# Optimization experiments

Hardware: AMD Instinct MI355X
Metric: run time of the kernel (lower is better)

## Reference

```python
import jax, jax.numpy as jnp
import numpy as np

K = 4
EDGE_NUM = 8978
SLOPE = 0.33


def _add_self_loops(ei, w, n):
    # add_self_loops(..., fill_value=-1.0); inputs assumed already coalesced
    loop = jnp.arange(n, dtype=ei.dtype)
    src = jnp.concatenate([ei[0], loop])
    dst = jnp.concatenate([ei[1], loop])
    w = jnp.concatenate([w, jnp.full((n,), -1.0, w.dtype)])
    return src, dst, w


def _cheb_bn_lrelu(x, src, dst, w, theta, bias, gamma, beta):
    # HodgeChebConv (PyG ChebConv recurrence) + BatchNorm + LeakyReLU; dropout = eval/no-op
    n = x.shape[0]

    def prop(z):  # y[dst] += w * z[src]
        return jax.ops.segment_sum(w[:, None] * z[src], dst, num_segments=n)

    Tx0 = x
    out = jnp.einsum('ni,io->no', Tx0, theta[0])
    Tx1 = prop(Tx0)
    out = out + jnp.einsum('ni,io->no', Tx1, theta[1])
    for k in range(2, K):
        Tx2 = 2.0 * prop(Tx1) - Tx0
        out = out + jnp.einsum('ni,io->no', Tx2, theta[k])
        Tx0, Tx1 = Tx1, Tx2
    out = out + bias
    mu = out.mean(0)
    var = out.var(0)
    out = (out - mu) * jax.lax.rsqrt(var + 1e-5) * gamma + beta
    return jnp.where(out >= 0, out, SLOPE * out)


def _bn(x, g, b):
    mu = x.mean(0)
    var = x.var(0)
    return (x - mu) * jax.lax.rsqrt(var + 1e-5) * g + b


def setup_inputs() -> dict:
    key = jax.random.key(0)
    ks = jax.random.split(key, 16)
    f32 = jnp.float32
    B = 64
    N = B * EDGE_NUM
    N2 = N // 2
    E = N * 8
    E1 = N2 * 8
    inp = {}
    inp['x_s'] = jax.random.normal(ks[0], (N, 1), f32)
    inp['edge_index_s'] = jax.random.randint(ks[1], (2, E), 0, N)
    inp['edge_weight_s'] = jax.random.normal(ks[2], (E,), f32) * 0.1
    inp['edge_index_s1'] = jax.random.randint(ks[3], (2, E1), 0, N2)
    inp['edge_weight_s1'] = jax.random.normal(ks[4], (E1,), f32) * 0.1
    # graclus-style pairing of node matchings (deterministic stand-in)
    inp['cluster'] = jnp.arange(N, dtype=jnp.int32) // 2
    inp['theta0'] = jax.random.normal(ks[5], (K, 1, 32), f32) * 0.1
    inp['bias0'] = jnp.zeros((32,), f32)
    inp['gamma0'] = jnp.ones((32,), f32)
    inp['beta0'] = jnp.zeros((32,), f32)
    inp['theta1'] = jax.random.normal(ks[6], (K, 32, 32), f32) * 0.1
    inp['bias1'] = jnp.zeros((32,), f32)
    inp['gamma1'] = jnp.ones((32,), f32)
    inp['beta1'] = jnp.zeros((32,), f32)
    inp['theta2'] = jax.random.normal(ks[7], (K, 32, 1), f32) * 0.1
    inp['bias2'] = jnp.zeros((1,), f32)
    inp['gamma2'] = jnp.ones((1,), f32)
    inp['beta2'] = jnp.zeros((1,), f32)
    LIN_IN = EDGE_NUM // 2  # 4489
    inp['W1'] = jax.random.normal(ks[8], (LIN_IN, 256), f32) * 0.02
    inp['b1'] = jnp.zeros((256,), f32)
    inp['g1'] = jnp.ones((256,), f32)
    inp['be1'] = jnp.zeros((256,), f32)
    inp['W2'] = jax.random.normal(ks[9], (256, 128), f32) * 0.05
    inp['b2'] = jnp.zeros((128,), f32)
    inp['g2'] = jnp.ones((128,), f32)
    inp['be2'] = jnp.zeros((128,), f32)
    inp['W3'] = jax.random.normal(ks[10], (128, 1), f32) * 0.05
    inp['b3'] = jnp.zeros((1,), f32)
    return inp


def reference(x_s, edge_weight_s, edge_weight_s1, theta0, bias0, gamma0, beta0,
              theta1, bias1, gamma1, beta1, theta2, bias2, gamma2, beta2,
              W1, b1, g1, be1, W2, b2, g2, be2, W3, b3,
              edge_index_s, edge_index_s1, cluster):
    n = x_s.shape[0]
    batch = n // EDGE_NUM
    n2 = n // 2
    src, dst, w = _add_self_loops(edge_index_s, edge_weight_s, n)
    x = _cheb_bn_lrelu(x_s, src, dst, w, theta0, bias0, gamma0, beta0)
    # Graclus max-pool with externally supplied cluster assignment + pooled graph
    x = jax.ops.segment_max(x, cluster, num_segments=n2)
    src1, dst1, w1 = _add_self_loops(edge_index_s1, edge_weight_s1, n2)
    x = _cheb_bn_lrelu(x, src1, dst1, w1, theta1, bias1, gamma1, beta1)
    x = _cheb_bn_lrelu(x, src1, dst1, w1, theta2, bias2, gamma2, beta2)
    x = x.reshape(batch, -1)  # [B, edge_num/2] since last channel = 1
    x = jax.nn.relu(_bn(x @ W1 + b1, g1, be1))
    x = jax.nn.relu(_bn(x @ W2 + b2, g2, be2))
    return x @ W3 + b3
```

## Files before the change

kernel.cpp:

```cpp
#include <hip/hip_runtime.h>

#define TPB 256
#define PBLK 512
#define BSH 12
#define BKT 4096
#define PCH 2048

__global__ __launch_bounds__(256) void bcount_k(const int* __restrict__ dst,
                                                int* __restrict__ bcnt, int NB, int E) {
  __shared__ int h[256];
  int tid = threadIdx.x;
  h[tid] = 0;
  __syncthreads();
  int stride = gridDim.x * 256;
  for (int e = blockIdx.x * 256 + tid; e < E; e += stride) atomicAdd(&h[dst[e] >> BSH], 1);
  __syncthreads();
  if (tid < NB && h[tid]) atomicAdd(&bcnt[tid], h[tid]);
}

__global__ void bscan_k(const int* __restrict__ bcnt, int* __restrict__ bbase,
                        int* __restrict__ bcur, int NB) {
  __shared__ int ls[256];
  int tid = threadIdx.x;
  int v = (tid < NB) ? bcnt[tid] : 0;
  ls[tid] = v;
  __syncthreads();
  for (int off = 1; off < 256; off <<= 1) {
    int t = (tid >= off) ? ls[tid - off] : 0;
    __syncthreads();
    ls[tid] += t;
    __syncthreads();
  }
  if (tid < NB) {
    bbase[tid] = ls[tid] - v;
    bcur[tid] = ls[tid] - v;
  }
}

__global__ __launch_bounds__(256) void bpart_k(const int* __restrict__ src,
                                               const int* __restrict__ dst,
                                               const float* __restrict__ w, int* __restrict__ gcur,
                                               int* __restrict__ psrc, int* __restrict__ pw,
                                               int* __restrict__ pdst, int NB, int E) {
  __shared__ int hist[256], start[256], resv[256], lcur[256];
  __shared__ int s_src[PCH], s_w[PCH], s_dst[PCH];
  __shared__ int total;
  int tid = threadIdx.x;
  int base = blockIdx.x * PCH;
  hist[tid] = 0;
  __syncthreads();
  int es[8], ds[8], wsv[8], bs[8];
#pragma unroll
  for (int i = 0; i < 8; ++i) {
    int e = base + i * 256 + tid;
    bool v = e < E;
    ds[i] = v ? dst[e] : 0;
    es[i] = v ? src[e] : 0;
    wsv[i] = v ? __float_as_int(w[e]) : 0;
    bs[i] = v ? (ds[i] >> BSH) : -1;
    if (v) atomicAdd(&hist[bs[i]], 1);
  }
  __syncthreads();
  int hv = hist[tid];
  start[tid] = hv;
  __syncthreads();
  for (int off = 1; off < 256; off <<= 1) {
    int t = (tid >= off) ? start[tid - off] : 0;
    __syncthreads();
    start[tid] += t;
    __syncthreads();
  }
  int ex = start[tid] - hv;
  __syncthreads();
  start[tid] = ex;
  lcur[tid] = ex;
  if (tid == 255) total = ex + hv;
  if (tid < NB && hv) resv[tid] = atomicAdd(&gcur[tid], hv);
  __syncthreads();
#pragma unroll
  for (int i = 0; i < 8; ++i) {
    if (bs[i] >= 0) {
      int p = atomicAdd(&lcur[bs[i]], 1);
      s_src[p] = es[i];
      s_w[p] = wsv[i];
      s_dst[p] = ds[i];
    }
  }
  __syncthreads();
  int m = total;
  for (int i = tid; i < m; i += 256) {
    int d = s_dst[i];
    int b = d >> BSH;
    int g = resv[b] + (i - start[b]);
    psrc[g] = s_src[i];
    pw[g] = s_w[i];
    pdst[g] = d;
  }
}

__global__ __launch_bounds__(1024) void bbuild_k(const int* __restrict__ psrc,
                                                 const int* __restrict__ pw,
                                                 const int* __restrict__ pdst,
                                                 const int* __restrict__ bbase,
                                                 const int* __restrict__ bcnt,
                                                 int* __restrict__ rowptr, int2* __restrict__ csw,
                                                 int n, int NB, int Etot) {
  __shared__ int hist[BKT];
  __shared__ int cur[BKT];
  __shared__ int aux[1024];
  int tid = threadIdx.x;
  int b = blockIdx.x;
  int node0 = b << BSH;
  int nn = min(BKT, n - node0);
  for (int i = tid; i < BKT; i += 1024) hist[i] = 0;
  __syncthreads();
  int ebase = bbase[b], ecnt = bcnt[b];
  for (int i = tid; i < ecnt; i += 1024) atomicAdd(&hist[pdst[ebase + i] - node0], 1);
  __syncthreads();
  int h0 = hist[tid * 4], h1 = hist[tid * 4 + 1], h2 = hist[tid * 4 + 2], h3 = hist[tid * 4 + 3];
  int s = h0 + h1 + h2 + h3;
  aux[tid] = s;
  __syncthreads();
  for (int off = 1; off < 1024; off <<= 1) {
    int t = (tid >= off) ? aux[tid - off] : 0;
    __syncthreads();
    aux[tid] += t;
    __syncthreads();
  }
  int ex = aux[tid] - s;
  hist[tid * 4] = ex;
  hist[tid * 4 + 1] = ex + h0;
  hist[tid * 4 + 2] = ex + h0 + h1;
  hist[tid * 4 + 3] = ex + h0 + h1 + h2;
  cur[tid * 4] = ex;
  cur[tid * 4 + 1] = ex + h0;
  cur[tid * 4 + 2] = ex + h0 + h1;
  cur[tid * 4 + 3] = ex + h0 + h1 + h2;
  __syncthreads();
  for (int j = tid; j < nn; j += 1024) rowptr[node0 + j] = ebase + hist[j];
  if (b == NB - 1 && tid == 0) rowptr[n] = Etot;
  for (int i = tid; i < ecnt; i += 1024) {
    int d = pdst[ebase + i] - node0;
    int p = atomicAdd(&cur[d], 1);
    csw[ebase + p] = make_int2(psrc[ebase + i], pw[ebase + i]);
  }
}

__global__ __launch_bounds__(256) void gather_s_k(float* __restrict__ out,
                                                  const float* __restrict__ z,
                                                  const float* __restrict__ bsub, float cb,
                                                  const int* __restrict__ rowptr,
                                                  const int2* __restrict__ csw, float scale,
                                                  int n) {
  int t = blockIdx.x * TPB + threadIdx.x;
  int node = t >> 3, q = t & 7;
  if (node >= n) return;
  int beg = rowptr[node], deg = rowptr[node + 1] - beg;
  float part = 0.f;
  for (int jb = 0; jb < deg; jb += 8) {
    int j = jb + q;
    int2 e = csw[beg + (j < deg ? j : 0)];
    int sj = (j < deg) ? e.x : 0;
    float zv = z[sj];
    part += (j < deg) ? __int_as_float(e.y) * zv : 0.f;
  }
  part += __shfl_xor(part, 1, 8);
  part += __shfl_xor(part, 2, 8);
  part += __shfl_xor(part, 4, 8);
  if (q == 0) out[node] = scale * (part - z[node]) + cb * bsub[node];
}

__global__ __launch_bounds__(256) void cheb0_fused_k(float4* __restrict__ out,
                                                     const float* __restrict__ x,
                                                     const float* __restrict__ t1,
                                                     const float* __restrict__ t2,
                                                     const int* __restrict__ rowptr,
                                                     const int2* __restrict__ csw,
                                                     const float* __restrict__ th ,
                                                     const float* __restrict__ bias, int n) {
  int t = blockIdx.x * TPB + threadIdx.x;
  int node = t >> 3, q = t & 7;
  if (node >= n) return;
  int beg = rowptr[node], deg = rowptr[node + 1] - beg;
  float part = 0.f;
  for (int jb = 0; jb < deg; jb += 8) {
    int j = jb + q;
    int2 e = csw[beg + (j < deg ? j : 0)];
    int sj = (j < deg) ? e.x : 0;
    float zv = t2[sj];
    part += (j < deg) ? __int_as_float(e.y) * zv : 0.f;
  }
  part += __shfl_xor(part, 1, 8);
  part += __shfl_xor(part, 2, 8);
  part += __shfl_xor(part, 4, 8);
  float t2n = t2[node], t1n = t1[node], xn = x[node];
  float t3 = 2.f * (part - t2n) - t1n;
  const float4* th4 = (const float4*)th;
  float4 a0 = th4[q], a1 = th4[8 + q], a2 = th4[16 + q], a3 = th4[24 + q];
  float4 b = ((const float4*)bias)[q];
  float4 r;
  r.x = xn * a0.x + t1n * a1.x + t2n * a2.x + t3 * a3.x + b.x;
  r.y = xn * a0.y + t1n * a1.y + t2n * a2.y + t3 * a3.y + b.y;
  r.z = xn * a0.z + t1n * a1.z + t2n * a2.z + t3 * a3.z + b.z;
  r.w = xn * a0.w + t1n * a1.w + t2n * a2.w + t3 * a3.w + b.w;
  out[(size_t)node * 8 + q] = r;
}

__device__ __forceinline__ float4 gather_row8(const float4* __restrict__ z,
                                              const int* __restrict__ rowptr,
                                              const int2* __restrict__ csw, int node, int q) {
  int beg = rowptr[node], deg = rowptr[node + 1] - beg;
  int full = min(deg, 8);
  int2 e = csw[beg + (q < deg ? q : 0)];
  int sj[8];
  float wj[8];
#pragma unroll
  for (int j = 0; j < 8; ++j) {
    int s = __shfl(e.x, j, 8);
    float w = __int_as_float(__shfl(e.y, j, 8));
    sj[j] = (j < full) ? s : 0;
    wj[j] = (j < full) ? w : 0.f;
  }
  float4 v[8];
#pragma unroll
  for (int j = 0; j < 8; ++j) v[j] = z[(size_t)sj[j] * 8 + q];
  float4 acc = {0.f, 0.f, 0.f, 0.f};
#pragma unroll
  for (int j = 0; j < 8; ++j) {
    acc.x = fmaf(wj[j], v[j].x, acc.x);
    acc.y = fmaf(wj[j], v[j].y, acc.y);
    acc.z = fmaf(wj[j], v[j].z, acc.z);
    acc.w = fmaf(wj[j], v[j].w, acc.w);
  }
  for (int j = 8; j < deg; ++j) {
    int2 ee = csw[beg + j];
    float w = __int_as_float(ee.y);
    float4 vv = z[(size_t)ee.x * 8 + q];
    acc.x = fmaf(w, vv.x, acc.x);
    acc.y = fmaf(w, vv.y, acc.y);
    acc.z = fmaf(w, vv.z, acc.z);
    acc.w = fmaf(w, vv.w, acc.w);
  }
  return acc;
}

__global__ __launch_bounds__(256) void gather_v32_k(float4* __restrict__ out,
                                                    const float4* __restrict__ z,
                                                    const float4* __restrict__ bsub, float cb,
                                                    const int* __restrict__ rowptr,
                                                    const int2* __restrict__ csw, float scale,
                                                    int n) {
  int t = blockIdx.x * TPB + threadIdx.x;
  int node = t >> 3, q = t & 7;
  if (node >= n) return;
  float4 acc = gather_row8(z, rowptr, csw, node, q);
  float4 zn = z[(size_t)node * 8 + q];
  float4 r;
  r.x = scale * (acc.x - zn.x);
  r.y = scale * (acc.y - zn.y);
  r.z = scale * (acc.z - zn.z);
  r.w = scale * (acc.w - zn.w);
  if (cb != 0.f) {
    float4 bs = bsub[(size_t)node * 8 + q];
    r.x = fmaf(cb, bs.x, r.x);
    r.y = fmaf(cb, bs.y, r.y);
    r.z = fmaf(cb, bs.z, r.z);
    r.w = fmaf(cb, bs.w, r.w);
  }
  out[(size_t)node * 8 + q] = r;
}

__global__ __launch_bounds__(256) void cheb32_fused_k(
    float4* __restrict__ out, const float4* __restrict__ x0, const float4* __restrict__ x1,
    const float4* __restrict__ x2, const int* __restrict__ rowptr, const int2* __restrict__ csw,
    const float* __restrict__ th , const float* __restrict__ bias, int n) {
  __shared__ float sth[4096];
  __shared__ float sx[4][32][36];
  int tid = threadIdx.x;
  for (int i = tid; i < 4096; i += 256) sth[i] = th[i];
  int t = blockIdx.x * TPB + tid;
  int node = t >> 3, q = t & 7, ln = tid >> 3;
  if (node < n) {
    float4 acc = gather_row8(x2, rowptr, csw, node, q);
    float4 tb = x2[(size_t)node * 8 + q];
    float4 ta = x1[(size_t)node * 8 + q];
    float4 xi = x0[(size_t)node * 8 + q];
    float4 tc;
    tc.x = 2.f * (acc.x - tb.x) - ta.x;
    tc.y = 2.f * (acc.y - tb.y) - ta.y;
    tc.z = 2.f * (acc.z - tb.z) - ta.z;
    tc.w = 2.f * (acc.w - tb.w) - ta.w;
    *(float4*)&sx[0][ln][q * 4] = xi;
    *(float4*)&sx[1][ln][q * 4] = ta;
    *(float4*)&sx[2][ln][q * 4] = tb;
    *(float4*)&sx[3][ln][q * 4] = tc;
  }
  __syncthreads();
  if (node < n) {
    float4 r = ((const float4*)bias)[q];
#pragma unroll
    for (int k = 0; k < 4; ++k) {
      const float* xr = sx[k][ln];
      const float* tr = &sth[k * 1024 + q * 4];
#pragma unroll
      for (int i = 0; i < 32; ++i) {
        float xv = xr[i];
        float4 tv = *(const float4*)&tr[i * 32];
        r.x = fmaf(xv, tv.x, r.x);
        r.y = fmaf(xv, tv.y, r.y);
        r.z = fmaf(xv, tv.z, r.z);
        r.w = fmaf(xv, tv.w, r.w);
      }
    }
    out[(size_t)node * 8 + q] = r;
  }
}

__global__ __launch_bounds__(256) void cheb1_fused_k(
    float* __restrict__ out, const float4* __restrict__ x0, const float4* __restrict__ x1,
    const float4* __restrict__ x2, const int* __restrict__ rowptr, const int2* __restrict__ csw,
    const float* __restrict__ th , const float* __restrict__ bias, int n) {
  int t = blockIdx.x * TPB + threadIdx.x;
  int node = t >> 3, q = t & 7;
  if (node >= n) return;
  float4 acc = gather_row8(x2, rowptr, csw, node, q);
  float4 tb = x2[(size_t)node * 8 + q];
  float4 ta = x1[(size_t)node * 8 + q];
  float4 xi = x0[(size_t)node * 8 + q];
  float4 tc;
  tc.x = 2.f * (acc.x - tb.x) - ta.x;
  tc.y = 2.f * (acc.y - tb.y) - ta.y;
  tc.z = 2.f * (acc.z - tb.z) - ta.z;
  tc.w = 2.f * (acc.w - tb.w) - ta.w;
  const float4* th4 = (const float4*)th;
  float4 h0 = th4[q], h1 = th4[8 + q], h2 = th4[16 + q], h3 = th4[24 + q];
  float p = xi.x * h0.x + xi.y * h0.y + xi.z * h0.z + xi.w * h0.w;
  p += ta.x * h1.x + ta.y * h1.y + ta.z * h1.z + ta.w * h1.w;
  p += tb.x * h2.x + tb.y * h2.y + tb.z * h2.z + tb.w * h2.w;
  p += tc.x * h3.x + tc.y * h3.y + tc.z * h3.z + tc.w * h3.w;
  p += __shfl_xor(p, 1);
  p += __shfl_xor(p, 2);
  p += __shfl_xor(p, 4);
  if (q == 0) out[node] = p + bias[0];
}

__global__ void bnlr_pool_k(float* __restrict__ y, const float* __restrict__ x,
                            const float* __restrict__ mv, const float* __restrict__ g,
                            const float* __restrict__ be, int n2c, float slope) {
  int i = blockIdx.x * TPB + threadIdx.x;
  if (i < n2c) {
    int p = i >> 5, c = i & 31;
    float sc = mv[32 + c] * g[c];
    float sh = be[c] - mv[c] * sc;
    float a = x[(size_t)(2 * p) * 32 + c] * sc + sh;
    float b = x[(size_t)(2 * p + 1) * 32 + c] * sc + sh;
    a = a >= 0.f ? a : slope * a;
    b = b >= 0.f ? b : slope * b;
    y[i] = fmaxf(a, b);
  }
}

__global__ __launch_bounds__(256) void stats_k(const float* __restrict__ x,
                                               float* __restrict__ partial, int C, int total) {
  float s = 0.f, q = 0.f;
  int stride = gridDim.x * TPB;
  for (int i = blockIdx.x * TPB + threadIdx.x; i < total; i += stride) {
    float v = x[i];
    s += v;
    q += v * v;
  }
  __shared__ float ss[256], sq[256];
  int tid = threadIdx.x;
  ss[tid] = s;
  sq[tid] = q;
  __syncthreads();
  for (int st = 128; st >= C; st >>= 1) {
    if (tid < st) {
      ss[tid] += ss[tid + st];
      sq[tid] += sq[tid + st];
    }
    __syncthreads();
  }
  if (tid < C) {
    partial[blockIdx.x * 2 * C + tid] = ss[tid];
    partial[blockIdx.x * 2 * C + C + tid] = sq[tid];
  }
}

__global__ __launch_bounds__(1024) void stats_fin_k(const float* __restrict__ partial,
                                                    float* __restrict__ mv, int C, int nblk,
                                                    float invR) {
  __shared__ float ss[1024], sq[1024];
  int tid = threadIdx.x;
  int G = 1024 / C;
  int g = tid / C, c = tid - g * C;
  float s = 0.f, q = 0.f;
  for (int b = g; b < nblk; b += G) {
    s += partial[b * 2 * C + c];
    q += partial[b * 2 * C + C + c];
  }
  ss[tid] = s;
  sq[tid] = q;
  __syncthreads();
  for (int st = 512; st >= C; st >>= 1) {
    if (tid < st) {
      ss[tid] += ss[tid + st];
      sq[tid] += sq[tid + st];
    }
    __syncthreads();
  }
  if (tid < C) {
    float mu = ss[tid] * invR;
    float var = sq[tid] * invR - mu * mu;
    mv[tid] = mu;
    mv[C + tid] = rsqrtf(var + 1e-5f);
  }
}

__global__ void bn_lrelu_k(float* __restrict__ y, const float* __restrict__ mv,
                           const float* __restrict__ g, const float* __restrict__ be, int C,
                           int total, float slope) {
  int i = blockIdx.x * TPB + threadIdx.x;
  if (i < total) {
    int c = i & (C - 1);
    float v = (y[i] - mv[c]) * mv[C + c] * g[c] + be[c];
    y[i] = v >= 0.f ? v : slope * v;
  }
}

__global__ void mlp1_init_k(float* __restrict__ h, const float* __restrict__ bias) {
  int i = blockIdx.x * TPB + threadIdx.x;
  h[i] = bias[i & 255];
}

#define MS 32
__global__ __launch_bounds__(256) void mlp1_split_k(const float* __restrict__ x,
                                                    const float* __restrict__ W,
                                                    float* __restrict__ h, int LIN) {
  int bb = blockIdx.x * 8;
  int s = blockIdx.y;
  int chunk = (LIN + MS - 1) / MS;
  int k0 = s * chunk;
  int k1 = min(k0 + chunk, LIN);
  __shared__ float sx[8][144];
  for (int i = threadIdx.x; i < 8 * chunk; i += 256) {
    int r = i / chunk, k = i - r * chunk;
    sx[r][k] = (k0 + k < LIN) ? x[(size_t)(bb + r) * LIN + k0 + k] : 0.f;
  }
  __syncthreads();
  int o = threadIdx.x;
  float acc[8] = {0.f, 0.f, 0.f, 0.f, 0.f, 0.f, 0.f, 0.f};
  for (int k = k0; k < k1; ++k) {
    float wv = W[(size_t)k * 256 + o];
#pragma unroll
    for (int r = 0; r < 8; ++r) acc[r] = fmaf(sx[r][k - k0], wv, acc[r]);
  }
#pragma unroll
  for (int r = 0; r < 8; ++r) unsafeAtomicAdd(&h[(bb + r) * 256 + o], acc[r]);
}

__global__ void bn_relu64_k(float* __restrict__ h, const float* __restrict__ g,
                            const float* __restrict__ be, int C, int R) {
  int c = blockIdx.x * blockDim.x + threadIdx.x;
  if (c < C) {
    float s = 0.f, q = 0.f;
    for (int r = 0; r < R; ++r) {
      float v = h[r * C + c];
      s += v;
      q += v * v;
    }
    float mu = s / R;
    float inv = rsqrtf(q / R - mu * mu + 1e-5f);
    for (int r = 0; r < R; ++r) {
      float v = (h[r * C + c] - mu) * inv * g[c] + be[c];
      h[r * C + c] = v > 0.f ? v : 0.f;
    }
  }
}

__global__ void mlp2_k(const float* __restrict__ x, const float* __restrict__ W,
                       const float* __restrict__ bias, float* __restrict__ h, int IN, int OUT) {
  __shared__ float sx[256];
  int b = blockIdx.x;
  for (int i = threadIdx.x; i < IN; i += blockDim.x) sx[i] = x[b * IN + i];
  __syncthreads();
  int o = threadIdx.x;
  if (o < OUT) {
    float acc = 0.f;
    for (int i = 0; i < IN; ++i) acc = fmaf(sx[i], W[i * OUT + o], acc);
    h[b * OUT + o] = acc + bias[o];
  }
}

__global__ void mlp3_k(const float* __restrict__ x, const float* __restrict__ W,
                       const float* __restrict__ b3, float* __restrict__ out, int IN, int B) {
  int b = threadIdx.x;
  if (b < B) {
    float acc = 0.f;
    for (int i = 0; i < IN; ++i) acc = fmaf(x[b * IN + i], W[i], acc);
    out[b] = acc + b3[0];
  }
}

extern "C" void kernel_launch(void* const* d_in, const int* in_sizes, int n_in, void* d_out,
                              int out_size, void* d_ws, size_t ws_size, hipStream_t stream) {
  const float* x_s = (const float*)d_in[0];
  const int* ei = (const int*)d_in[1];
  const float* ew = (const float*)d_in[2];
  const int* ei1 = (const int*)d_in[3];
  const float* ew1 = (const float*)d_in[4];
  const float* th0 = (const float*)d_in[6];
  const float* cb0 = (const float*)d_in[7];
  const float* g0 = (const float*)d_in[8];
  const float* be0 = (const float*)d_in[9];
  const float* th1 = (const float*)d_in[10];
  const float* cb1 = (const float*)d_in[11];
  const float* g1c = (const float*)d_in[12];
  const float* be1c = (const float*)d_in[13];
  const float* th2 = (const float*)d_in[14];
  const float* cb2 = (const float*)d_in[15];
  const float* g2c = (const float*)d_in[16];
  const float* be2c = (const float*)d_in[17];
  const float* W1 = (const float*)d_in[18];
  const float* mb1 = (const float*)d_in[19];
  const float* mg1 = (const float*)d_in[20];
  const float* mbe1 = (const float*)d_in[21];
  const float* W2 = (const float*)d_in[22];
  const float* mb2 = (const float*)d_in[23];
  const float* mg2 = (const float*)d_in[24];
  const float* mbe2 = (const float*)d_in[25];
  const float* W3 = (const float*)d_in[26];
  const float* mb3 = (const float*)d_in[27];
  float* outp = (float*)d_out;

  const int N = in_sizes[0];
  const int E = in_sizes[2];
  const int N2 = N / 2;
  const int E1 = in_sizes[4];
  const int B = out_size;
  const int LIN = N2 / B;
  const size_t NC = (size_t)N * 32, N2C = (size_t)N2 * 32;

  const int* srcA = ei;
  const int* dstA = ei + E;
  const int* src1 = ei1;
  const int* dst1 = ei1 + E1;

  float* ws = (float*)d_ws;
  float* OUT0 = ws;
  float* X1 = OUT0 + NC;
  float* TA = X1 + N2C;
  float* TB = TA + N2C;
  float* OUT1 = TB + N2C;
  int* deg1 = (int*)(OUT1 + N2C);
  int* rowptr1 = deg1 + N2;
  int2* csw1 = (int2*)(rowptr1 + N2 + 2);
  float* partial = (float*)(csw1 + E1);
  float* mv = partial + PBLK * 64;
  int* bcnt = (int*)(mv + 64);
  int* bbase = bcnt + 256;
  int* bcur = bbase + 256;
  float* h1 = (float*)(bcur + 256);
  float* h2 = h1 + (size_t)B * 256;
  int* psrc = (int*)OUT0;
  int* pw = psrc + E;
  int* pdst = pw + E;
  int2* csw0 = (int2*)X1;
  float* t1 = TA;
  int* rowptr0 = (int*)TA + N;
  float* t2 = TB;
  float* OUT2 = X1;

  auto cdiv = [](long long a, long long b) { return (unsigned)((a + b - 1) / b); };
  int NB0 = (int)cdiv(N, BKT), NB1 = (int)cdiv(N2, BKT);

  hipMemsetAsync(bcnt, 0, 256 * 4, stream);
  bcount_k<<<1024, 256, 0, stream>>>(dstA, bcnt, NB0, E);
  bscan_k<<<1, 256, 0, stream>>>(bcnt, bbase, bcur, NB0);
  bpart_k<<<cdiv(E, PCH), 256, 0, stream>>>(srcA, dstA, ew, bcur, psrc, pw, pdst, NB0, E);
  bbuild_k<<<NB0, 1024, 0, stream>>>(psrc, pw, pdst, bbase, bcnt, rowptr0, csw0, N, NB0, E);

  hipMemsetAsync(bcnt, 0, 256 * 4, stream);
  bcount_k<<<1024, 256, 0, stream>>>(dst1, bcnt, NB1, E1);
  bscan_k<<<1, 256, 0, stream>>>(bcnt, bbase, bcur, NB1);
  bpart_k<<<cdiv(E1, PCH), 256, 0, stream>>>(src1, dst1, ew1, bcur, psrc, pw, pdst, NB1, E1);
  bbuild_k<<<NB1, 1024, 0, stream>>>(psrc, pw, pdst, bbase, bcnt, rowptr1, csw1, N2, NB1, E1);

  gather_s_k<<<cdiv((long long)N * 8, TPB), TPB, 0, stream>>>(t1, x_s, x_s, 0.f, rowptr0, csw0,
                                                              1.f, N);
  gather_s_k<<<cdiv((long long)N * 8, TPB), TPB, 0, stream>>>(t2, t1, x_s, -1.f, rowptr0, csw0,
                                                              2.f, N);
  cheb0_fused_k<<<cdiv((long long)N * 8, TPB), TPB, 0, stream>>>((float4*)OUT0, x_s, t1, t2,
                                                                 rowptr0, csw0, th0, cb0, N);
  stats_k<<<PBLK, TPB, 0, stream>>>(OUT0, partial, 32, (int)NC);
  stats_fin_k<<<1, 1024, 0, stream>>>(partial, mv, 32, PBLK, 1.f / N);
  bnlr_pool_k<<<cdiv(N2C, TPB), TPB, 0, stream>>>(X1, OUT0, mv, g0, be0, (int)N2C, 0.33f);

  unsigned g = cdiv((long long)N2 * 8, TPB);
  gather_v32_k<<<g, TPB, 0, stream>>>((float4*)TA, (const float4*)X1, (const float4*)X1, 0.f,
                                      rowptr1, csw1, 1.f, N2);
  gather_v32_k<<<g, TPB, 0, stream>>>((float4*)TB, (const float4*)TA, (const float4*)X1, -1.f,
                                      rowptr1, csw1, 2.f, N2);
  cheb32_fused_k<<<g, TPB, 0, stream>>>((float4*)OUT1, (const float4*)X1, (const float4*)TA,
                                        (const float4*)TB, rowptr1, csw1, th1, cb1, N2);
  stats_k<<<PBLK, TPB, 0, stream>>>(OUT1, partial, 32, (int)N2C);
  stats_fin_k<<<1, 1024, 0, stream>>>(partial, mv, 32, PBLK, 1.f / N2);
  bn_lrelu_k<<<cdiv(N2C, TPB), TPB, 0, stream>>>(OUT1, mv, g1c, be1c, 32, (int)N2C, 0.33f);

  gather_v32_k<<<g, TPB, 0, stream>>>((float4*)TA, (const float4*)OUT1, (const float4*)OUT1, 0.f,
                                      rowptr1, csw1, 1.f, N2);
  gather_v32_k<<<g, TPB, 0, stream>>>((float4*)TB, (const float4*)TA, (const float4*)OUT1, -1.f,
                                      rowptr1, csw1, 2.f, N2);
  cheb1_fused_k<<<g, TPB, 0, stream>>>(OUT2, (const float4*)OUT1, (const float4*)TA,
                                       (const float4*)TB, rowptr1, csw1, th2, cb2, N2);
  stats_k<<<PBLK, TPB, 0, stream>>>(OUT2, partial, 1, N2);
  stats_fin_k<<<1, 1024, 0, stream>>>(partial, mv, 1, PBLK, 1.f / N2);
  bn_lrelu_k<<<cdiv(N2, TPB), TPB, 0, stream>>>(OUT2, mv, g2c, be2c, 1, N2, 0.33f);

  mlp1_init_k<<<cdiv((long long)B * 256, TPB), TPB, 0, stream>>>(h1, mb1);
  mlp1_split_k<<<dim3(B / 8, MS), 256, 0, stream>>>(OUT2, W1, h1, LIN);
  bn_relu64_k<<<1, 256, 0, stream>>>(h1, mg1, mbe1, 256, B);
  mlp2_k<<<B, 128, 0, stream>>>(h1, W2, mb2, h2, 256, 128);
  bn_relu64_k<<<1, 128, 0, stream>>>(h2, mg2, mbe2, 128, B);
  mlp3_k<<<1, 64, 0, stream>>>(h2, W3, mb3, outp, 128, B);
}
```

Baseline: 1.096 ms.

## Gather 32-channel neighbor features from fp16 shadow copies in Chebyshev propagation

Producers of the 32-channel node features (pool, BN+LeakyReLU, gather kernels) now also write an fp16 shadow copy. The random-index neighbor gathers in the Chebyshev recurrences read these half-precision rows and accumulate in fp32, halving the bytes moved by the scattered loads. The cost is an extra fp16 store per producer and lower precision in the propagated features, which may affect accuracy tolerance. Shadow buffers are aliased into scratch regions (OUT0, TB), which requires those regions to be free at that point.

```diff
diff --git a/kernel.cpp b/kernel.cpp
--- a/kernel.cpp
+++ b/kernel.cpp
@@ -1,4 +1,5 @@
 #include <hip/hip_runtime.h>
+#include <hip/hip_fp16.h>
 
 #define TPB 256
 #define PBLK 512
@@ -206,9 +207,9 @@
   out[(size_t)node * 8 + q] = r;
 }
 
-__device__ __forceinline__ float4 gather_row8(const float4* __restrict__ z,
-                                              const int* __restrict__ rowptr,
-                                              const int2* __restrict__ csw, int node, int q) {
+__device__ __forceinline__ float4 gather_row8h(const uint2* __restrict__ zh,
+                                               const int* __restrict__ rowptr,
+                                               const int2* __restrict__ csw, int node, int q) {
   int beg = rowptr[node], deg = rowptr[node + 1] - beg;
   int full = min(deg, 8);
   int2 e = csw[beg + (q < deg ? q : 0)];
@@ -221,39 +222,50 @@
     sj[j] = (j < full) ? s : 0;
     wj[j] = (j < full) ? w : 0.f;
   }
-  float4 v[8];
-#pragma unroll
-  for (int j = 0; j < 8; ++j) v[j] = z[(size_t)sj[j] * 8 + q];
+  uint2 v[8];
+#pragma unroll
+  for (int j = 0; j < 8; ++j) v[j] = zh[(size_t)sj[j] * 8 + q];
   float4 acc = {0.f, 0.f, 0.f, 0.f};
 #pragma unroll
   for (int j = 0; j < 8; ++j) {
-    acc.x = fmaf(wj[j], v[j].x, acc.x);
-    acc.y = fmaf(wj[j], v[j].y, acc.y);
-    acc.z = fmaf(wj[j], v[j].z, acc.z);
-    acc.w = fmaf(wj[j], v[j].w, acc.w);
+    float2 a = __half22float2(*(const __half2*)&v[j].x);
+    float2 b = __half22float2(*(const __half2*)&v[j].y);
+    acc.x = fmaf(wj[j], a.x, acc.x);
+    acc.y = fmaf(wj[j], a.y, acc.y);
+    acc.z = fmaf(wj[j], b.x, acc.z);
+    acc.w = fmaf(wj[j], b.y, acc.w);
   }
   for (int j = 8; j < deg; ++j) {
     int2 ee = csw[beg + j];
     float w = __int_as_float(ee.y);
-    float4 vv = z[(size_t)ee.x * 8 + q];
-    acc.x = fmaf(w, vv.x, acc.x);
-    acc.y = fmaf(w, vv.y, acc.y);
-    acc.z = fmaf(w, vv.z, acc.z);
-    acc.w = fmaf(w, vv.w, acc.w);
+    uint2 vv = zh[(size_t)ee.x * 8 + q];
+    float2 a = __half22float2(*(const __half2*)&vv.x);
+    float2 b = __half22float2(*(const __half2*)&vv.y);
+    acc.x = fmaf(w, a.x, acc.x);
+    acc.y = fmaf(w, a.y, acc.y);
+    acc.z = fmaf(w, b.x, acc.z);
+    acc.w = fmaf(w, b.y, acc.w);
   }
   return acc;
 }
 
-__global__ __launch_bounds__(256) void gather_v32_k(float4* __restrict__ out,
-                                                    const float4* __restrict__ z,
-                                                    const float4* __restrict__ bsub, float cb,
-                                                    const int* __restrict__ rowptr,
-                                                    const int2* __restrict__ csw, float scale,
-                                                    int n) {
+__device__ __forceinline__ uint2 pack_h4(float4 r) {
+  __half2 p0 = __float22half2_rn(make_float2(r.x, r.y));
+  __half2 p1 = __float22half2_rn(make_float2(r.z, r.w));
+  uint2 o;
+  o.x = *(const unsigned int*)&p0;
+  o.y = *(const unsigned int*)&p1;
+  return o;
+}
+
+__global__ __launch_bounds__(256) void gather_v32_k(
+    float4* __restrict__ out, uint2* __restrict__ outh, const float4* __restrict__ z,
+    const uint2* __restrict__ zh, const float4* __restrict__ bsub, float cb,
+    const int* __restrict__ rowptr, const int2* __restrict__ csw, float scale, int n) {
   int t = blockIdx.x * TPB + threadIdx.x;
   int node = t >> 3, q = t & 7;
   if (node >= n) return;
-  float4 acc = gather_row8(z, rowptr, csw, node, q);
+  float4 acc = gather_row8h(zh, rowptr, csw, node, q);
   float4 zn = z[(size_t)node * 8 + q];
   float4 r;
   r.x = scale * (acc.x - zn.x);
@@ -268,11 +280,13 @@
     r.w = fmaf(cb, bs.w, r.w);
   }
   out[(size_t)node * 8 + q] = r;
+  outh[(size_t)node * 8 + q] = pack_h4(r);
 }
 
 __global__ __launch_bounds__(256) void cheb32_fused_k(
     float4* __restrict__ out, const float4* __restrict__ x0, const float4* __restrict__ x1,
-    const float4* __restrict__ x2, const int* __restrict__ rowptr, const int2* __restrict__ csw,
+    const float4* __restrict__ x2, const uint2* __restrict__ x2h,
+    const int* __restrict__ rowptr, const int2* __restrict__ csw,
     const float* __restrict__ th , const float* __restrict__ bias, int n) {
   __shared__ float sth[4096];
   __shared__ float sx[4][32][36];
@@ -281,7 +295,7 @@
   int t = blockIdx.x * TPB + tid;
   int node = t >> 3, q = t & 7, ln = tid >> 3;
   if (node < n) {
-    float4 acc = gather_row8(x2, rowptr, csw, node, q);
+    float4 acc = gather_row8h(x2h, rowptr, csw, node, q);
     float4 tb = x2[(size_t)node * 8 + q];
     float4 ta = x1[(size_t)node * 8 + q];
     float4 xi = x0[(size_t)node * 8 + q];
@@ -318,12 +332,13 @@
 
 __global__ __launch_bounds__(256) void cheb1_fused_k(
     float* __restrict__ out, const float4* __restrict__ x0, const float4* __restrict__ x1,
-    const float4* __restrict__ x2, const int* __restrict__ rowptr, const int2* __restrict__ csw,
+    const float4* __restrict__ x2, const uint2* __restrict__ x2h,
+    const int* __restrict__ rowptr, const int2* __restrict__ csw,
     const float* __restrict__ th , const float* __restrict__ bias, int n) {
   int t = blockIdx.x * TPB + threadIdx.x;
   int node = t >> 3, q = t & 7;
   if (node >= n) return;
-  float4 acc = gather_row8(x2, rowptr, csw, node, q);
+  float4 acc = gather_row8h(x2h, rowptr, csw, node, q);
   float4 tb = x2[(size_t)node * 8 + q];
   float4 ta = x1[(size_t)node * 8 + q];
   float4 xi = x0[(size_t)node * 8 + q];
@@ -344,9 +359,10 @@
   if (q == 0) out[node] = p + bias[0];
 }
 
-__global__ void bnlr_pool_k(float* __restrict__ y, const float* __restrict__ x,
-                            const float* __restrict__ mv, const float* __restrict__ g,
-                            const float* __restrict__ be, int n2c, float slope) {
+__global__ void bnlr_pool_k(float* __restrict__ y, __half* __restrict__ yh,
+                            const float* __restrict__ x, const float* __restrict__ mv,
+                            const float* __restrict__ g, const float* __restrict__ be, int n2c,
+                            float slope) {
   int i = blockIdx.x * TPB + threadIdx.x;
   if (i < n2c) {
     int p = i >> 5, c = i & 31;
@@ -356,7 +372,9 @@
     float b = x[(size_t)(2 * p + 1) * 32 + c] * sc + sh;
     a = a >= 0.f ? a : slope * a;
     b = b >= 0.f ? b : slope * b;
-    y[i] = fmaxf(a, b);
+    float r = fmaxf(a, b);
+    y[i] = r;
+    yh[i] = __float2half(r);
   }
 }
 
@@ -417,14 +435,16 @@
   }
 }
 
-__global__ void bn_lrelu_k(float* __restrict__ y, const float* __restrict__ mv,
-                           const float* __restrict__ g, const float* __restrict__ be, int C,
-                           int total, float slope) {
+__global__ void bn_lrelu_k(float* __restrict__ y, __half* __restrict__ yh,
+                           const float* __restrict__ mv, const float* __restrict__ g,
+                           const float* __restrict__ be, int C, int total, float slope) {
   int i = blockIdx.x * TPB + threadIdx.x;
   if (i < total) {
     int c = i & (C - 1);
     float v = (y[i] - mv[c]) * mv[C + c] * g[c] + be[c];
-    y[i] = v >= 0.f ? v : slope * v;
+    v = v >= 0.f ? v : slope * v;
+    y[i] = v;
+    if (yh) yh[i] = __float2half(v);
   }
 }
 
@@ -570,6 +590,10 @@
   int* rowptr0 = (int*)TA + N;
   float* t2 = TB;
   float* OUT2 = X1;
+  uint2* TAh = (uint2*)OUT0;
+  uint2* TBh = (uint2*)(OUT0 + N2C / 2);
+  uint2* O1h = (uint2*)(OUT0 + N2C);
+  __half* X1h = (__half*)TB;
 
   auto cdiv = [](long long a, long long b) { return (unsigned)((a + b - 1) / b); };
   int NB0 = (int)cdiv(N, BKT), NB1 = (int)cdiv(N2, BKT);
@@ -594,28 +618,30 @@
                                                                  rowptr0, csw0, th0, cb0, N);
   stats_k<<<PBLK, TPB, 0, stream>>>(OUT0, partial, 32, (int)NC);
   stats_fin_k<<<1, 1024, 0, stream>>>(partial, mv, 32, PBLK, 1.f / N);
-  bnlr_pool_k<<<cdiv(N2C, TPB), TPB, 0, stream>>>(X1, OUT0, mv, g0, be0, (int)N2C, 0.33f);
+  bnlr_pool_k<<<cdiv(N2C, TPB), TPB, 0, stream>>>(X1, X1h, OUT0, mv, g0, be0, (int)N2C, 0.33f);
 
   unsigned g = cdiv((long long)N2 * 8, TPB);
-  gather_v32_k<<<g, TPB, 0, stream>>>((float4*)TA, (const float4*)X1, (const float4*)X1, 0.f,
-                                      rowptr1, csw1, 1.f, N2);
-  gather_v32_k<<<g, TPB, 0, stream>>>((float4*)TB, (const float4*)TA, (const float4*)X1, -1.f,
-                                      rowptr1, csw1, 2.f, N2);
+  gather_v32_k<<<g, TPB, 0, stream>>>((float4*)TA, TAh, (const float4*)X1, (const uint2*)X1h,
+                                      (const float4*)X1, 0.f, rowptr1, csw1, 1.f, N2);
+  gather_v32_k<<<g, TPB, 0, stream>>>((float4*)TB, TBh, (const float4*)TA, TAh,
+                                      (const float4*)X1, -1.f, rowptr1, csw1, 2.f, N2);
   cheb32_fused_k<<<g, TPB, 0, stream>>>((float4*)OUT1, (const float4*)X1, (const float4*)TA,
-                                        (const float4*)TB, rowptr1, csw1, th1, cb1, N2);
+                                        (const float4*)TB, TBh, rowptr1, csw1, th1, cb1, N2);
   stats_k<<<PBLK, TPB, 0, stream>>>(OUT1, partial, 32, (int)N2C);
   stats_fin_k<<<1, 1024, 0, stream>>>(partial, mv, 32, PBLK, 1.f / N2);
-  bn_lrelu_k<<<cdiv(N2C, TPB), TPB, 0, stream>>>(OUT1, mv, g1c, be1c, 32, (int)N2C, 0.33f);
-
-  gather_v32_k<<<g, TPB, 0, stream>>>((float4*)TA, (const float4*)OUT1, (const float4*)OUT1, 0.f,
-                                      rowptr1, csw1, 1.f, N2);
-  gather_v32_k<<<g, TPB, 0, stream>>>((float4*)TB, (const float4*)TA, (const float4*)OUT1, -1.f,
-                                      rowptr1, csw1, 2.f, N2);
+  bn_lrelu_k<<<cdiv(N2C, TPB), TPB, 0, stream>>>(OUT1, (__half*)O1h, mv, g1c, be1c, 32, (int)N2C,
+                                                 0.33f);
+
+  gather_v32_k<<<g, TPB, 0, stream>>>((float4*)TA, TAh, (const float4*)OUT1, O1h,
+                                      (const float4*)OUT1, 0.f, rowptr1, csw1, 1.f, N2);
+  gather_v32_k<<<g, TPB, 0, stream>>>((float4*)TB, TBh, (const float4*)TA, TAh,
+                                      (const float4*)OUT1, -1.f, rowptr1, csw1, 2.f, N2);
   cheb1_fused_k<<<g, TPB, 0, stream>>>(OUT2, (const float4*)OUT1, (const float4*)TA,
-                                       (const float4*)TB, rowptr1, csw1, th2, cb2, N2);
+                                       (const float4*)TB, TBh, rowptr1, csw1, th2, cb2, N2);
   stats_k<<<PBLK, TPB, 0, stream>>>(OUT2, partial, 1, N2);
   stats_fin_k<<<1, 1024, 0, stream>>>(partial, mv, 1, PBLK, 1.f / N2);
-  bn_lrelu_k<<<cdiv(N2, TPB), TPB, 0, stream>>>(OUT2, mv, g2c, be2c, 1, N2, 0.33f);
+  bn_lrelu_k<<<cdiv(N2, TPB), TPB, 0, stream>>>(OUT2, (__half*)nullptr, mv, g2c, be2c, 1, N2,
+                                                0.33f);
 
   mlp1_init_k<<<cdiv((long long)B * 256, TPB), TPB, 0, stream>>>(h1, mb1);
   mlp1_split_k<<<dim3(B / 8, MS), 256, 0, stream>>>(OUT2, W1, h1, LIN);
```

Result: no change. 1.098 ms (+0.2%).
